# Optimization experiments

Measured on AMD Instinct MI355X. Metric: run time of the kernel, lower is better.

## Reference

```python
import jax, jax.numpy as jnp
import numpy as np

B, S, HID, NH, HD, SKV = 2, 2048, 1024, 16, 64, 2048

def setup_inputs() -> dict:
    key = jax.random.key(0)
    ks = jax.random.split(key, 9)
    s = 0.02
    return {
        "hidden_states": jax.random.normal(ks[0], (B, S, HID), jnp.float32),
        "kvs": jax.random.normal(ks[1], (2, B, NH, SKV, HD), jnp.float32),
        "Wq": jax.random.normal(ks[2], (HID, HID), jnp.float32) * s,
        "bq": jax.random.normal(ks[3], (HID,), jnp.float32) * s,
        "Wk": jax.random.normal(ks[4], (HID, HID), jnp.float32) * s,
        "bk": jax.random.normal(ks[5], (HID,), jnp.float32) * s,
        "Wv": jax.random.normal(ks[6], (HID, HID), jnp.float32) * s,
        "bv": jax.random.normal(ks[7], (HID,), jnp.float32) * s,
        "kv_weight": jnp.ones((), jnp.float32),
    }

def _heads(x):
    # [B,S,HID] -> [B,NH,S,HD]
    return x.reshape(B, -1, NH, HD).transpose(0, 2, 1, 3)

def reference(hidden_states, kvs, Wq, bq, Wk, bk, Wv, bv, kv_weight):
    scale = HD ** (-0.5)
    # torch nn.Linear: y = x @ W.T + b
    q = _heads((hidden_states @ Wq.T + bq) * scale)        # [B,NH,S,HD]
    k = _heads(hidden_states @ Wk.T + bk)
    v = _heads(hidden_states @ Wv.T + bv)
    k = jnp.concatenate([kv_weight * kvs[0], k], axis=2)   # [B,NH,SKV+S,HD]
    v = jnp.concatenate([kv_weight * kvs[1], v], axis=2)
    # module scales twice: q * d^-0.5 then scores / sqrt(d)
    scores = jnp.einsum("bhqd,bhkd->bhqk", q, k) * scale
    probs = jax.nn.softmax(scores, axis=-1)
    # dropout(p=0.1) is identity in eval mode
    ctx = jnp.einsum("bhqk,bhkd->bhqd", probs, v)          # [B,NH,S,HD]
    ctx = ctx.transpose(0, 2, 1, 3).reshape(B, S, HID)
    return ctx
```

## Files before the change

kernel.cpp:

```cpp
#include <hip/hip_runtime.h>
#include <hip/hip_bf16.h>


typedef __bf16 bf16x8 __attribute__((ext_vector_type(8)));
typedef float f32x4 __attribute__((ext_vector_type(4)));
typedef float f32x16 __attribute__((ext_vector_type(16)));
typedef unsigned int uint4v __attribute__((ext_vector_type(4)));
typedef unsigned short u16x4 __attribute__((ext_vector_type(4)));

#define QSCALE 0.0225421100138900525f

static __device__ __forceinline__ unsigned short bf16b(float f) {
  return __builtin_bit_cast(unsigned short, __float2bfloat16(f));
}
static __device__ __forceinline__ unsigned pk2(float lo, float hi) {
  return (unsigned)bf16b(lo) | ((unsigned)bf16b(hi) << 16);
}
static __device__ __forceinline__ bf16x8 ld16s(const unsigned short* p) {
  return __builtin_bit_cast(bf16x8, *(const uint4v*)p);
}
static __device__ __forceinline__ float fexp2(float x) {
  float r; asm("v_exp_f32 %0, %1" : "=v"(r) : "v"(x)); return r;
}

typedef __attribute__((address_space(1))) const void gas_void;
typedef __attribute__((address_space(3))) void las_void;
static __device__ __forceinline__ void gload_lds16(const void* g, void* l) {
  __builtin_amdgcn_global_load_lds((gas_void*)g, (las_void*)l, 16, 0, 0);
}

__global__ __launch_bounds__(256) void prep_convert(
    const float* __restrict__ hs, const float* __restrict__ wq,
    const float* __restrict__ wk, const float* __restrict__ wv,
    const float* __restrict__ kv0, const float* __restrict__ kvw,
    unsigned short* __restrict__ hsb, unsigned short* __restrict__ wb,
    unsigned short* __restrict__ kbuf) {
  long i = ((long)blockIdx.x * 256 + threadIdx.x) * 4;
  const float* src; unsigned short* dst; float s = 1.0f;
  if (i < 4194304)      { src = hs + i;           dst = hsb + i; }
  else if (i < 5242880) { src = wq + (i-4194304); dst = wb + (i-4194304); }
  else if (i < 6291456) { src = wk + (i-5242880); dst = wb + 1048576 + (i-5242880); }
  else if (i < 7340032) { src = wv + (i-6291456); dst = wb + 2097152 + (i-6291456); }
  else { long j = i - 7340032; s = *kvw;
         long bh = j >> 17, r = j & 131071;
         src = kv0 + j; dst = kbuf + (bh << 18) + r; }
  float4 v = *(const float4*)src;
  u16x4 o = { bf16b(v.x*s), bf16b(v.y*s), bf16b(v.z*s), bf16b(v.w*s) };
  *(u16x4*)dst = o;
}

__global__ __launch_bounds__(256) void qkv_gemm(
    const unsigned short* __restrict__ A, const unsigned short* __restrict__ W,
    const float* __restrict__ bq, const float* __restrict__ bk, const float* __restrict__ bv,
    unsigned short* __restrict__ qb, unsigned short* __restrict__ kbuf,
    unsigned short* __restrict__ vtmp) {
  int mode = blockIdx.y;
  const unsigned short* Wm = W + mode * 1048576;
  const float* bias = (mode == 0) ? bq : ((mode == 1) ? bk : bv);
  int mt = blockIdx.x >> 3, nt = blockIdx.x & 7;
  int m0 = mt << 7, n0 = nt << 7;
  int wid = threadIdx.x >> 6, ln = threadIdx.x & 63;
  int wr = wid >> 1, wc = wid & 1;
  __shared__ unsigned short As[2][4096], Bs[2][4096];

  f32x4 acc[4][4] = {};

  auto stage = [&](int bb, int kt) {
    #pragma unroll
    for (int i = 0; i < 2; ++i) {
      int c = i*256 + wid*64 + ln;
      int row = c >> 2, sl = c & 3;
      int lb = (i*256 + wid*64) * 8;
      gload_lds16(A  + (long)(m0 + row)*1024 + kt*32 + sl*8, &As[bb][lb]);
      gload_lds16(Wm + (long)(n0 + row)*1024 + kt*32 + sl*8, &Bs[bb][lb]);
    }
  };

  stage(0, 0);
  __syncthreads();
  int buf = 0;
  for (int kt = 0; kt < 32; ++kt) {
    if (kt < 31) stage(buf ^ 1, kt + 1);
    bf16x8 a[4], b[4];
    int rsel = (ln & 15), ksel = (ln >> 4) * 8;
    #pragma unroll
    for (int x = 0; x < 4; ++x) {
      a[x] = ld16s(&As[buf][(wr*64 + x*16 + rsel)*32 + ksel]);
      b[x] = ld16s(&Bs[buf][(wc*64 + x*16 + rsel)*32 + ksel]);
    }
    __builtin_amdgcn_s_setprio(1);
    #pragma unroll
    for (int x = 0; x < 4; ++x)
      #pragma unroll
      for (int y = 0; y < 4; ++y)
        acc[x][y] = __builtin_amdgcn_mfma_f32_16x16x32_bf16(a[x], b[y], acc[x][y], 0, 0, 0);
    __builtin_amdgcn_s_setprio(0);
    __syncthreads();
    buf ^= 1;
  }

  float bias4[4];
  #pragma unroll
  for (int y = 0; y < 4; ++y) bias4[y] = bias[n0 + wc*64 + y*16 + (ln & 15)];

  #pragma unroll
  for (int x = 0; x < 4; ++x)
    #pragma unroll
    for (int y = 0; y < 4; ++y)
      #pragma unroll
      for (int r = 0; r < 4; ++r) {
        int gm = m0 + wr*64 + x*16 + (ln >> 4)*4 + r;
        int gn = n0 + wc*64 + y*16 + (ln & 15);
        float v = acc[x][y][r] + bias4[y];
        int bb = gm >> 11, s = gm & 2047, h = gn >> 6, d = gn & 63;
        long bh = bb*16 + h;
        if (mode == 0)      qb[(bh*2048 + s)*64 + d]        = bf16b(v * QSCALE);
        else if (mode == 1) kbuf[(bh*4096 + 2048 + s)*64 + d] = bf16b(v);
        else                vtmp[(bh*2048 + s)*64 + d]       = bf16b(v);
      }
}

template <typename T>
__global__ __launch_bounds__(256) void transpose_v(
    const T* __restrict__ src, unsigned short* __restrict__ dst,
    const float* __restrict__ scale_ptr, int col0) {
  __shared__ float tile[64 * 65];
  int bh = blockIdx.x >> 5;
  int s0 = (blockIdx.x & 31) << 6;
  int tid = threadIdx.x;
  float sc = scale_ptr ? *scale_ptr : 1.0f;
  long sb = ((long)bh*2048 + s0) * 64;
  if constexpr (sizeof(T) == 4) {
    #pragma unroll
    for (int j = 0; j < 4; ++j) {
      int c = tid + j*256;
      int row = c >> 4, sl = c & 15;
      float4 v = *(const float4*)(src + sb + row*64 + sl*4);
      float* p = &tile[row*65 + sl*4];
      p[0] = v.x*sc; p[1] = v.y*sc; p[2] = v.z*sc; p[3] = v.w*sc;
    }
  } else {
    #pragma unroll
    for (int j = 0; j < 2; ++j) {
      int c = tid + j*256;
      int row = c >> 3, sl = c & 7;
      uint4v u = *(const uint4v*)(src + sb + row*64 + sl*8);
      float* p = &tile[row*65 + sl*8];
      #pragma unroll
      for (int t = 0; t < 4; ++t) {
        unsigned w = u[t];
        p[2*t]   = __builtin_bit_cast(float, w << 16) * sc;
        p[2*t+1] = __builtin_bit_cast(float, w & 0xffff0000u) * sc;
      }
    }
  }
  __syncthreads();
  int d = tid >> 2, kc = tid & 3;
  unsigned short u16[16];
  #pragma unroll
  for (int t = 0; t < 16; ++t) u16[t] = bf16b(tile[(kc*16 + t)*65 + d]);
  uint4v o0v = { (unsigned)u16[0] | ((unsigned)u16[1]<<16), (unsigned)u16[2] | ((unsigned)u16[3]<<16),
                 (unsigned)u16[4] | ((unsigned)u16[5]<<16), (unsigned)u16[6] | ((unsigned)u16[7]<<16) };
  uint4v o1v = { (unsigned)u16[8] | ((unsigned)u16[9]<<16), (unsigned)u16[10] | ((unsigned)u16[11]<<16),
                 (unsigned)u16[12] | ((unsigned)u16[13]<<16), (unsigned)u16[14] | ((unsigned)u16[15]<<16) };
  long db = (long)bh*262144 + (long)d*4096 + col0 + s0 + kc*16;
  *(uint4v*)(dst + db) = o0v;
  *(uint4v*)(dst + db + 8) = o1v;
}

template <int NT, bool DIRECT>
__global__ __launch_bounds__(256) void attn(
    const unsigned short* __restrict__ qb, const unsigned short* __restrict__ kb,
    const unsigned short* __restrict__ vtb, float* __restrict__ out,
    float* __restrict__ po, float* __restrict__ pl) {
  int tilei = blockIdx.x, bh = blockIdx.y, sp = blockIdx.z;
  int keyoff = sp * NT * 64;
  int wid = threadIdx.x >> 6, ln = threadIdx.x & 63;
  int lo = ln & 31, hi = ln >> 5;
  __shared__ unsigned short Ks[2][4096], Vs[2][4096];

  const unsigned short* kg = kb  + (long)bh * 262144;
  const unsigned short* vg = vtb + (long)bh * 262144;
  int q = tilei*128 + wid*32 + lo;
  const unsigned short* qrow = qb + ((long)bh*2048 + q) * 64;
  bf16x8 qf[4];
  #pragma unroll
  for (int ds = 0; ds < 4; ++ds) qf[ds] = ld16s(qrow + ds*16 + hi*8);

  f32x16 o0 = {}, o1 = {};
  f32x16 lacc = {};

  auto stage = [&](int bb, int t) {
    int key0 = keyoff + (t << 6);
    #pragma unroll
    for (int i = 0; i < 2; ++i) {
      int c = i*256 + wid*64 + ln;
      int row = c >> 3, sl = c & 7;
      int swz = (sl ^ (row & 7)) * 8;
      int lb = (i*256 + wid*64) * 8;
      gload_lds16(kg + (long)(key0 + row)*64 + swz, &Ks[bb][lb]);
      gload_lds16(vg + (long)row*4096 + key0 + swz, &Vs[bb][lb]);
    }
  };

  stage(0, 0);
  __syncthreads();
  int buf = 0;
  for (int t = 0; t < NT; ++t) {
    if (t < NT-1) stage(buf ^ 1, t + 1);
    const unsigned short* Kt = Ks[buf];
    const unsigned short* Vt = Vs[buf];
    #pragma unroll
    for (int cc = 0; cc < 2; ++cc) {
      f32x16 st = {};
      int key = cc*32 + lo;
      __builtin_amdgcn_s_setprio(1);
      #pragma unroll
      for (int ds = 0; ds < 4; ++ds) {
        int sl = ((2*ds + hi) ^ (key & 7)) * 8;
        bf16x8 kf = ld16s(&Kt[key*64 + sl]);
        st = __builtin_amdgcn_mfma_f32_32x32x16_bf16(kf, qf[ds], st, 0, 0, 0);
      }
      __builtin_amdgcn_s_setprio(0);
      float p[16];
      #pragma unroll
      for (int r = 0; r < 16; ++r) p[r] = fexp2(st[r]);
      #pragma unroll
      for (int r = 0; r < 16; ++r) lacc[r] += p[r];
      #pragma unroll
      for (int ks = 0; ks < 2; ++ks) {
        unsigned X  = pk2(p[8*ks+0], p[8*ks+1]);
        unsigned X2 = pk2(p[8*ks+2], p[8*ks+3]);
        unsigned Y  = pk2(p[8*ks+4], p[8*ks+5]);
        unsigned Y2 = pk2(p[8*ks+6], p[8*ks+7]);
        asm("v_permlane32_swap_b32 %0, %1" : "+v"(X), "+v"(Y));
        asm("v_permlane32_swap_b32 %0, %1" : "+v"(X2), "+v"(Y2));
        uint4v pw = { X, X2, Y, Y2 };
        bf16x8 pf = __builtin_bit_cast(bf16x8, pw);
        int slv = ((cc*4 + 2*ks + hi) ^ (lo & 7)) * 8;
        bf16x8 vf0 = ld16s(&Vt[lo*64 + slv]);
        bf16x8 vf1 = ld16s(&Vt[(32 + lo)*64 + slv]);
        __builtin_amdgcn_s_setprio(1);
        o0 = __builtin_amdgcn_mfma_f32_32x32x16_bf16(vf0, pf, o0, 0, 0, 0);
        o1 = __builtin_amdgcn_mfma_f32_32x32x16_bf16(vf1, pf, o1, 0, 0, 0);
        __builtin_amdgcn_s_setprio(0);
      }
    }
    __syncthreads();
    buf ^= 1;
  }

  float lsum = ((lacc[0]+lacc[1]) + (lacc[2]+lacc[3])) + ((lacc[4]+lacc[5]) + (lacc[6]+lacc[7]))
             + ((lacc[8]+lacc[9]) + (lacc[10]+lacc[11])) + ((lacc[12]+lacc[13]) + (lacc[14]+lacc[15]));
  lsum += __shfl_xor(lsum, 32, 64);

  if constexpr (DIRECT) {
    float inv = 1.0f / lsum;
    int bb = bh >> 4, h = bh & 15;
    float* orow = out + ((long)bb*2048 + q)*1024 + h*64;
    #pragma unroll
    for (int dh = 0; dh < 2; ++dh) {
      f32x16 oo = dh ? o1 : o0;
      #pragma unroll
      for (int g = 0; g < 4; ++g) {
        f32x4 vv = { oo[4*g]*inv, oo[4*g+1]*inv, oo[4*g+2]*inv, oo[4*g+3]*inv };
        *(f32x4*)(orow + dh*32 + g*8 + 4*hi) = vv;
      }
    }
  } else {
    float* prow = po + (((long)sp*32 + bh)*2048 + q) * 64;
    #pragma unroll
    for (int dh = 0; dh < 2; ++dh) {
      f32x16 oo = dh ? o1 : o0;
      #pragma unroll
      for (int g = 0; g < 4; ++g) {
        f32x4 vv = { oo[4*g], oo[4*g+1], oo[4*g+2], oo[4*g+3] };
        *(f32x4*)(prow + dh*32 + g*8 + 4*hi) = vv;
      }
    }
    if (hi == 0) pl[((long)sp*32 + bh)*2048 + q] = lsum;
  }
}

__global__ __launch_bounds__(256) void combine2(
    const float* __restrict__ po, const float* __restrict__ pl, float* __restrict__ out) {
  long flat = ((long)blockIdx.x * 256 + threadIdx.x) * 4;
  int bh = (int)(flat >> 17);
  int rem = (int)(flat & 131071);
  int q = rem >> 6, d = rem & 63;
  f32x4 a = *(const f32x4*)(po + flat);
  f32x4 b = *(const f32x4*)(po + 4194304 + flat);
  float l = pl[bh*2048 + q] + pl[65536 + bh*2048 + q];
  float inv = 1.0f / l;
  f32x4 r = { (a[0]+b[0])*inv, (a[1]+b[1])*inv, (a[2]+b[2])*inv, (a[3]+b[3])*inv };
  *(f32x4*)(out + ((long)(bh >> 4)*2048 + q)*1024 + (bh & 15)*64 + d) = r;
}

extern "C" void kernel_launch(void* const* d_in, const int* in_sizes, int n_in,
                              void* d_out, int out_size, void* d_ws, size_t ws_size,
                              hipStream_t stream) {
  const float* hs  = (const float*)d_in[0];
  const float* kvs = (const float*)d_in[1];
  const float* Wq  = (const float*)d_in[2];
  const float* bq  = (const float*)d_in[3];
  const float* Wk  = (const float*)d_in[4];
  const float* bk  = (const float*)d_in[5];
  const float* Wv  = (const float*)d_in[6];
  const float* bv  = (const float*)d_in[7];
  const float* kvw = (const float*)d_in[8];
  float* out = (float*)d_out;

  char* w = (char*)d_ws;
  unsigned short* hsb  = (unsigned short*)(w);
  unsigned short* wb   = (unsigned short*)(w + (8l  << 20));
  unsigned short* qbuf = (unsigned short*)(w + (14l << 20));
  unsigned short* kbuf = (unsigned short*)(w + (22l << 20));
  unsigned short* vtb  = (unsigned short*)(w + (38l << 20));
  unsigned short* vtmp = (unsigned short*)(w + (54l << 20));
  float* po = (float*)(w + (64l << 20));
  float* pl = (float*)(w + (128l << 20));

  const float* kv0 = kvs;
  const float* kv1 = kvs + 4194304;

  prep_convert<<<dim3(11264), dim3(256), 0, stream>>>(hs, Wq, Wk, Wv, kv0, kvw, hsb, wb, kbuf);
  qkv_gemm<<<dim3(256, 3), dim3(256), 0, stream>>>(hsb, wb, bq, bk, bv, qbuf, kbuf, vtmp);
  transpose_v<float><<<dim3(1024), dim3(256), 0, stream>>>(kv1, vtb, kvw, 0);
  transpose_v<unsigned short><<<dim3(1024), dim3(256), 0, stream>>>(vtmp, vtb, (const float*)nullptr, 2048);

  if (ws_size >= (129ul << 20)) {
    attn<32, false><<<dim3(16, 32, 2), dim3(256), 0, stream>>>(qbuf, kbuf, vtb, nullptr, po, pl);
    combine2<<<dim3(4096), dim3(256), 0, stream>>>(po, pl, out);
  } else {
    attn<64, true><<<dim3(16, 32, 1), dim3(256), 0, stream>>>(qbuf, kbuf, vtb, out, nullptr, nullptr);
  }
}
```

Before: 261.6 us.

## Process two 32-query groups per wave to reuse K/V LDS fragments

Each wave now handles 64 query rows (two 32-row groups) instead of 32, so every K fragment and V fragment loaded from LDS feeds two MFMAs. The query tile per block doubles to 256, which halves the grid and the total K/V staging traffic. In exchange, register pressure rises (four output accumulators plus two query fragment sets), and fewer blocks are available to fill the 256 CUs.

```diff
diff --git a/kernel.cpp b/kernel.cpp
--- a/kernel.cpp
+++ b/kernel.cpp
@@ -181,14 +181,17 @@
 
   const unsigned short* kg = kb  + (long)bh * 262144;
   const unsigned short* vg = vtb + (long)bh * 262144;
-  int q = tilei*128 + wid*32 + lo;
-  const unsigned short* qrow = qb + ((long)bh*2048 + q) * 64;
-  bf16x8 qf[4];
-  #pragma unroll
-  for (int ds = 0; ds < 4; ++ds) qf[ds] = ld16s(qrow + ds*16 + hi*8);
-
-  f32x16 o0 = {}, o1 = {};
-  f32x16 lacc = {};
+  int qbase = tilei*256 + wid*64;
+  bf16x8 qf[2][4];
+  #pragma unroll
+  for (int g = 0; g < 2; ++g) {
+    const unsigned short* qrow = qb + ((long)bh*2048 + qbase + g*32 + lo) * 64;
+    #pragma unroll
+    for (int ds = 0; ds < 4; ++ds) qf[g][ds] = ld16s(qrow + ds*16 + hi*8);
+  }
+
+  f32x16 o[2][2] = {};
+  f32x4 lacc[2] = {};
 
   auto stage = [&](int bb, int t) {
     int key0 = keyoff + (t << 6);
@@ -212,37 +215,49 @@
     const unsigned short* Vt = Vs[buf];
     #pragma unroll
     for (int cc = 0; cc < 2; ++cc) {
-      f32x16 st = {};
       int key = cc*32 + lo;
-      __builtin_amdgcn_s_setprio(1);
-      #pragma unroll
-      for (int ds = 0; ds < 4; ++ds) {
-        int sl = ((2*ds + hi) ^ (key & 7)) * 8;
-        bf16x8 kf = ld16s(&Kt[key*64 + sl]);
-        st = __builtin_amdgcn_mfma_f32_32x32x16_bf16(kf, qf[ds], st, 0, 0, 0);
-      }
-      __builtin_amdgcn_s_setprio(0);
-      float p[16];
-      #pragma unroll
-      for (int r = 0; r < 16; ++r) p[r] = fexp2(st[r]);
-      #pragma unroll
-      for (int r = 0; r < 16; ++r) lacc[r] += p[r];
+      bf16x8 kf[4];
+      #pragma unroll
+      for (int ds = 0; ds < 4; ++ds)
+        kf[ds] = ld16s(&Kt[key*64 + ((2*ds + hi) ^ (key & 7))*8]);
+      bf16x8 pf[2][2];
+      #pragma unroll
+      for (int g = 0; g < 2; ++g) {
+        f32x16 st = {};
+        __builtin_amdgcn_s_setprio(1);
+        #pragma unroll
+        for (int ds = 0; ds < 4; ++ds)
+          st = __builtin_amdgcn_mfma_f32_32x32x16_bf16(kf[ds], qf[g][ds], st, 0, 0, 0);
+        __builtin_amdgcn_s_setprio(0);
+        float p[16];
+        #pragma unroll
+        for (int r = 0; r < 16; ++r) p[r] = fexp2(st[r]);
+        f32x4 l4 = { (p[0]+p[1]) + (p[2]+p[3]),   (p[4]+p[5]) + (p[6]+p[7]),
+                     (p[8]+p[9]) + (p[10]+p[11]), (p[12]+p[13]) + (p[14]+p[15]) };
+        lacc[g] += l4;
+        #pragma unroll
+        for (int ks = 0; ks < 2; ++ks) {
+          unsigned X  = pk2(p[8*ks+0], p[8*ks+1]);
+          unsigned X2 = pk2(p[8*ks+2], p[8*ks+3]);
+          unsigned Y  = pk2(p[8*ks+4], p[8*ks+5]);
+          unsigned Y2 = pk2(p[8*ks+6], p[8*ks+7]);
+          asm("v_permlane32_swap_b32 %0, %1" : "+v"(X), "+v"(Y));
+          asm("v_permlane32_swap_b32 %0, %1" : "+v"(X2), "+v"(Y2));
+          uint4v pw = { X, X2, Y, Y2 };
+          pf[g][ks] = __builtin_bit_cast(bf16x8, pw);
+        }
+      }
       #pragma unroll
       for (int ks = 0; ks < 2; ++ks) {
-        unsigned X  = pk2(p[8*ks+0], p[8*ks+1]);
-        unsigned X2 = pk2(p[8*ks+2], p[8*ks+3]);
-        unsigned Y  = pk2(p[8*ks+4], p[8*ks+5]);
-        unsigned Y2 = pk2(p[8*ks+6], p[8*ks+7]);
-        asm("v_permlane32_swap_b32 %0, %1" : "+v"(X), "+v"(Y));
-        asm("v_permlane32_swap_b32 %0, %1" : "+v"(X2), "+v"(Y2));
-        uint4v pw = { X, X2, Y, Y2 };
-        bf16x8 pf = __builtin_bit_cast(bf16x8, pw);
         int slv = ((cc*4 + 2*ks + hi) ^ (lo & 7)) * 8;
         bf16x8 vf0 = ld16s(&Vt[lo*64 + slv]);
         bf16x8 vf1 = ld16s(&Vt[(32 + lo)*64 + slv]);
         __builtin_amdgcn_s_setprio(1);
-        o0 = __builtin_amdgcn_mfma_f32_32x32x16_bf16(vf0, pf, o0, 0, 0, 0);
-        o1 = __builtin_amdgcn_mfma_f32_32x32x16_bf16(vf1, pf, o1, 0, 0, 0);
+        #pragma unroll
+        for (int g = 0; g < 2; ++g) {
+          o[g][0] = __builtin_amdgcn_mfma_f32_32x32x16_bf16(vf0, pf[g][ks], o[g][0], 0, 0, 0);
+          o[g][1] = __builtin_amdgcn_mfma_f32_32x32x16_bf16(vf1, pf[g][ks], o[g][1], 0, 0, 0);
+        }
         __builtin_amdgcn_s_setprio(0);
       }
     }
@@ -250,35 +265,36 @@
     buf ^= 1;
   }
 
-  float lsum = ((lacc[0]+lacc[1]) + (lacc[2]+lacc[3])) + ((lacc[4]+lacc[5]) + (lacc[6]+lacc[7]))
-             + ((lacc[8]+lacc[9]) + (lacc[10]+lacc[11])) + ((lacc[12]+lacc[13]) + (lacc[14]+lacc[15]));
-  lsum += __shfl_xor(lsum, 32, 64);
-
-  if constexpr (DIRECT) {
-    float inv = 1.0f / lsum;
-    int bb = bh >> 4, h = bh & 15;
-    float* orow = out + ((long)bb*2048 + q)*1024 + h*64;
-    #pragma unroll
-    for (int dh = 0; dh < 2; ++dh) {
-      f32x16 oo = dh ? o1 : o0;
-      #pragma unroll
-      for (int g = 0; g < 4; ++g) {
-        f32x4 vv = { oo[4*g]*inv, oo[4*g+1]*inv, oo[4*g+2]*inv, oo[4*g+3]*inv };
-        *(f32x4*)(orow + dh*32 + g*8 + 4*hi) = vv;
-      }
-    }
-  } else {
-    float* prow = po + (((long)sp*32 + bh)*2048 + q) * 64;
-    #pragma unroll
-    for (int dh = 0; dh < 2; ++dh) {
-      f32x16 oo = dh ? o1 : o0;
-      #pragma unroll
-      for (int g = 0; g < 4; ++g) {
-        f32x4 vv = { oo[4*g], oo[4*g+1], oo[4*g+2], oo[4*g+3] };
-        *(f32x4*)(prow + dh*32 + g*8 + 4*hi) = vv;
-      }
-    }
-    if (hi == 0) pl[((long)sp*32 + bh)*2048 + q] = lsum;
+  #pragma unroll
+  for (int g = 0; g < 2; ++g) {
+    float lsum = (lacc[g][0] + lacc[g][1]) + (lacc[g][2] + lacc[g][3]);
+    lsum += __shfl_xor(lsum, 32, 64);
+    int q = qbase + g*32 + lo;
+    if constexpr (DIRECT) {
+      float inv = 1.0f / lsum;
+      int bb = bh >> 4, h = bh & 15;
+      float* orow = out + ((long)bb*2048 + q)*1024 + h*64;
+      #pragma unroll
+      for (int dh = 0; dh < 2; ++dh) {
+        #pragma unroll
+        for (int gg = 0; gg < 4; ++gg) {
+          f32x4 vv = { o[g][dh][4*gg]*inv, o[g][dh][4*gg+1]*inv,
+                       o[g][dh][4*gg+2]*inv, o[g][dh][4*gg+3]*inv };
+          *(f32x4*)(orow + dh*32 + gg*8 + 4*hi) = vv;
+        }
+      }
+    } else {
+      float* prow = po + (((long)sp*32 + bh)*2048 + q) * 64;
+      #pragma unroll
+      for (int dh = 0; dh < 2; ++dh) {
+        #pragma unroll
+        for (int gg = 0; gg < 4; ++gg) {
+          f32x4 vv = { o[g][dh][4*gg], o[g][dh][4*gg+1], o[g][dh][4*gg+2], o[g][dh][4*gg+3] };
+          *(f32x4*)(prow + dh*32 + gg*8 + 4*hi) = vv;
+        }
+      }
+      if (hi == 0) pl[((long)sp*32 + bh)*2048 + q] = lsum;
+    }
   }
 }
 
@@ -329,9 +345,9 @@
   transpose_v<unsigned short><<<dim3(1024), dim3(256), 0, stream>>>(vtmp, vtb, (const float*)nullptr, 2048);
 
   if (ws_size >= (129ul << 20)) {
-    attn<32, false><<<dim3(16, 32, 2), dim3(256), 0, stream>>>(qbuf, kbuf, vtb, nullptr, po, pl);
+    attn<32, false><<<dim3(8, 32, 2), dim3(256), 0, stream>>>(qbuf, kbuf, vtb, nullptr, po, pl);
     combine2<<<dim3(4096), dim3(256), 0, stream>>>(po, pl, out);
   } else {
-    attn<64, true><<<dim3(16, 32, 1), dim3(256), 0, stream>>>(qbuf, kbuf, vtb, out, nullptr, nullptr);
-  }
-}
+    attn<64, true><<<dim3(8, 32, 1), dim3(256), 0, stream>>>(qbuf, kbuf, vtb, out, nullptr, nullptr);
+  }
+}
```

New measurement: 261.4 us. About the same (-0.1%).
